# Kernel optimization log

Hardware: AMD Instinct MI355X
Metric: run time of the kernel (lower is better)

## Reference

```python
import jax, jax.numpy as jnp
import numpy as np
from jax import lax

EPS = 1e-4  # BatchNorm2d eps
K, STRIDE, PAD = 3, 1, 1


def _conv_nchw(x, w, stride, pad):
    return lax.conv_general_dilated(
        x, w, window_strides=(stride, stride), padding=[(pad, pad), (pad, pad)],
        dimension_numbers=("NCHW", "OIHW", "NCHW"))


def setup_inputs() -> dict:
    key = jax.random.key(0)
    ks = jax.random.split(key, 6)
    N, C, H, W = 16, 256, 56, 56
    Cout = 256
    return {
        "x": jax.random.normal(ks[0], (N, C, H, W), jnp.float32),
        "bn_gamma": jax.random.uniform(ks[1], (C,), jnp.float32, 0.5, 1.5),
        "bn_beta": jax.random.normal(ks[2], (C,), jnp.float32) * 0.1,
        "conv_w": jax.random.normal(ks[3], (Cout, C, K, K), jnp.float32) * (1.0 / np.sqrt(C * K * K)),
        "conv_b": jax.random.normal(ks[4], (Cout,), jnp.float32) * 0.01,
        "beta_conv_b": jax.random.normal(ks[5], (1,), jnp.float32) * 0.01,
    }


def reference(x, bn_gamma, bn_beta, conv_w, conv_b, beta_conv_b):
    # --- BatchNorm2d (training-mode batch stats, affine) ---
    mean = jnp.mean(x, axis=(0, 2, 3), keepdims=True)
    var = jnp.mean(jnp.square(x - mean), axis=(0, 2, 3), keepdims=True)  # biased
    xn = (x - mean) * lax.rsqrt(var + EPS)
    xn = xn * bn_gamma[None, :, None, None] + bn_beta[None, :, None, None]

    # --- Ternary quantize (threshold=0; le overwrites ge, so x==0 -> -1) ---
    t = jnp.where(xn >= 0.0, 1.0, 0.0)
    t = jnp.where(xn <= 0.0, -1.0, t).astype(xn.dtype)
    # scale=True, clamp=True
    xc = jnp.clip(xn, -1.0, 1.0)
    c_sum = jnp.sum(xc * t, axis=1, keepdims=True)       # [N,1,H,W]
    c_cnt = jnp.sum(jnp.abs(t), axis=1, keepdims=True)   # L1 norm over channels

    # --- Main conv on ternary activations ---
    y = _conv_nchw(t, conv_w, STRIDE, PAD) + conv_b[None, :, None, None]

    # --- beta: ones-weight box filter (+ beta_conv bias) ---
    ones_k = jnp.ones((1, 1, K, K), x.dtype)
    b_sum = _conv_nchw(c_sum, ones_k, STRIDE, PAD) + beta_conv_b[0]
    b_cnt = _conv_nchw(c_cnt, ones_k, STRIDE, PAD) + beta_conv_b[0]
    beta_map = b_sum / b_cnt                             # [N,1,Ho,Wo]
    return y * beta_map
```

## Files before the change

### kernel.cpp

```cpp
#include <hip/hip_runtime.h>
#include <hip/hip_bf16.h>

typedef __attribute__((ext_vector_type(8))) short bf16x8;
typedef __attribute__((ext_vector_type(4))) float f32x4;

#define NB 16
#define C 256
#define HH 56
#define WW 56
#define HW 3136
#define CHW 802816
#define NPIX 50176
#define PH 58
#define PW 58
#define KTOT 2304

#define GLL(g, l) __builtin_amdgcn_global_load_lds( \
    (const __attribute__((address_space(1))) void*)(g), \
    (__attribute__((address_space(3))) void*)(l), 16, 0, 0)

__global__ void stats_kernel(const float* __restrict__ x, const float* __restrict__ gamma,
                             double* __restrict__ stats) {
  int c = blockIdx.x, tid = threadIdx.x;
  double s = 0.0, s2 = 0.0;
  const float* xc = x + (size_t)c * HW;
  for (int n = 0; n < NB; ++n) {
    const float4* xb = (const float4*)(xc + (size_t)n * CHW);
    for (int i = tid; i < HW / 4; i += 256) {
      float4 v = xb[i];
      double a = v.x, b = v.y, cc = v.z, d = v.w;
      s  += (a + b) + (cc + d);
      s2 += (a * a + b * b) + (cc * cc + d * d);
    }
  }
  __shared__ double rs[256], rq[256];
  rs[tid] = s; rq[tid] = s2; __syncthreads();
  for (int o = 128; o > 0; o >>= 1) {
    if (tid < o) { rs[tid] += rs[tid + o]; rq[tid] += rq[tid + o]; }
    __syncthreads();
  }
  if (tid == 0) {
    double mean = rs[0] / (double)NPIX;
    double var = rq[0] / (double)NPIX - mean * mean;
    stats[c] = mean;
    stats[C + c] = (double)gamma[c] / sqrt(var + 1e-4);
  }
}

__global__ __launch_bounds__(256) void ternarize_kernel(const float* __restrict__ x,
                                 const float* __restrict__ beta,
                                 const double* __restrict__ stats,
                                 unsigned short* __restrict__ Tp, float* __restrict__ csum) {
  int bid = blockIdx.x, tid = threadIdx.x;
  int n = bid / HH, h = bid - n * HH;
  __shared__ float xs[256][57];
  const float* xb = x + (size_t)n * CHW + h * WW;
#pragma unroll
  for (int j = 0; j < 14; ++j) {
    int idx = j * 256 + tid;
    int c = idx / 14, q = idx - c * 14;
    float4 v = *(const float4*)(xb + (size_t)c * HW + q * 4);
    float* row = &xs[c][q * 4];
    row[0] = v.x; row[1] = v.y; row[2] = v.z; row[3] = v.w;
  }
  int c8 = tid & 31;
  double mu[8], sc[8], bt[8];
#pragma unroll
  for (int e = 0; e < 8; ++e) {
    int c = c8 + 32 * e;
    mu[e] = stats[c]; sc[e] = stats[C + c]; bt[e] = (double)beta[c];
  }
  __syncthreads();
  unsigned short* tb = Tp + ((size_t)(n * PH + h + 1) * PW + 1) * C;
  float* cs = csum + (size_t)(n * PH + h + 1) * PW + 1;
#pragma unroll
  for (int p = 0; p < 7; ++p) {
    int idx = p * 256 + tid;
    int w = idx >> 5;
    unsigned bits[4];
    float msum = 0.f;
#pragma unroll
    for (int e2 = 0; e2 < 4; ++e2) {
      unsigned lo, hi;
      {
        double xn = ((double)xs[c8 + 64 * e2][w] - mu[2 * e2]) * sc[2 * e2] + bt[2 * e2];
        lo = (xn > 0.0) ? 0x3F80u : 0xBF80u;
        msum += (float)fmin(fabs(xn), 1.0);
      }
      {
        double xn = ((double)xs[c8 + 64 * e2 + 32][w] - mu[2 * e2 + 1]) * sc[2 * e2 + 1] + bt[2 * e2 + 1];
        hi = (xn > 0.0) ? 0x3F80u : 0xBF80u;
        msum += (float)fmin(fabs(xn), 1.0);
      }
      bits[e2] = lo | (hi << 16);
    }
    msum += __shfl_xor(msum, 1); msum += __shfl_xor(msum, 2);
    msum += __shfl_xor(msum, 4); msum += __shfl_xor(msum, 8);
    msum += __shfl_xor(msum, 16);
    uint4 v4; v4.x = bits[0]; v4.y = bits[1]; v4.z = bits[2]; v4.w = bits[3];
    *(uint4*)(tb + (size_t)w * C + c8 * 8) = v4;
    if (c8 == 0) cs[w] = msum;
  }
}

__global__ void border_kernel(unsigned short* __restrict__ Tp) {
  int g = blockIdx.x * 256 + threadIdx.x;
  if (g >= 16 * 228 * 32) return;
  int n = g / 7296; int r = g - n * 7296;
  int pix = r >> 5, c8 = r & 31;
  int h, w;
  if (pix < 58)      { h = 0;  w = pix; }
  else if (pix < 116){ h = 57; w = pix - 58; }
  else { int rem = pix - 116; h = 1 + (rem >> 1); w = (rem & 1) ? 57 : 0; }
  uint4 z = {0u, 0u, 0u, 0u};
  *(uint4*)(Tp + (size_t)((n * PH + h) * PW + w) * C + c8 * 8) = z;
}

__global__ void wprep_kernel(const float* __restrict__ cw, unsigned short* __restrict__ Wp) {
  int o = blockIdx.x * 256 + threadIdx.x;
  int co = o / KTOT, rr = o - co * KTOT;
  int tap = rr >> 8, p = rr & 255;
  int c = (p & 7) * 32 + (p >> 3);
  float v = cw[co * KTOT + c * 9 + tap];
  unsigned u = __builtin_bit_cast(unsigned, v);
  unsigned lsb = (u >> 16) & 1u;
  u += 0x7FFFu + lsb;
  Wp[o] = (unsigned short)(u >> 16);
}

__global__ void betamap_kernel(const float* __restrict__ csum, const float* __restrict__ betab,
                               float* __restrict__ bmap) {
  int idx = blockIdx.x * 256 + threadIdx.x;
  if (idx >= NPIX) return;
  int n = idx / HW, r = idx - n * HW;
  int h = r / WW, w = r - h * WW;
  const float* p = csum + (size_t)(n * PH + h) * PW + w;
  float s = 0.f;
  for (int i = 0; i < 3; ++i)
    for (int j = 0; j < 3; ++j) s += p[i * PW + j];
  int rows = 3 - (h == 0) - (h == HH - 1);
  int cols = 3 - (w == 0) - (w == WW - 1);
  float bb = betab[0];
  bmap[idx] = (s + bb) / (256.0f * (float)(rows * cols) + bb);
}

__global__ __launch_bounds__(256) void conv_kernel(const unsigned short* __restrict__ Wp,
    const unsigned short* __restrict__ Tp, const float* __restrict__ convb,
    const float* __restrict__ bmap, float* __restrict__ out) {
  int g = blockIdx.x;
  int gg = g >> 3, xcd = g & 7;
  int ct = gg & 1;
  int pt = (gg >> 1) * 8 + xcd;
  int pix0 = pt * 128, co0 = ct * 128;
  int tid = threadIdx.x;

  __shared__ __align__(16) unsigned short As[128 * 64];
  __shared__ __align__(16) unsigned short Bs[128 * 64];

  int jj = tid & 7;
  int rr_ = tid >> 3;
  int s = ((jj ^ (rr_ & 7)) * 8);

  const unsigned short* wA[4];
  const unsigned short* tB[4];
  unsigned short* dA[4];
  unsigned short* dB[4];
#pragma unroll
  for (int i = 0; i < 4; ++i) {
    int r = i * 32 + rr_;
    wA[i] = Wp + (size_t)(co0 + r) * KTOT + s;
    dA[i] = As + i * 2048 + tid * 8;
    int p = pix0 + r;
    int n = p / HW; int rm = p - n * HW; int h = rm / WW; int w = rm - h * WW;
    tB[i] = Tp + (size_t)((n * PH + h) * PW + w) * C + s;
    dB[i] = Bs + i * 2048 + tid * 8;
  }

  int lane = tid & 63, wid = tid >> 6;
  int wm = (wid >> 1) * 64, wn = (wid & 1) * 64;
  int quad = lane >> 4, row16 = lane & 15;
  int j0 = quad ^ (row16 & 7);
  const unsigned short* aB0 = As + (wm + row16) * 64 + j0 * 8;
  const unsigned short* aB1 = As + (wm + row16) * 64 + (j0 ^ 4) * 8;
  const unsigned short* bB0 = Bs + (wn + row16) * 64 + j0 * 8;
  const unsigned short* bB1 = Bs + (wn + row16) * 64 + (j0 ^ 4) * 8;

  f32x4 acc[4][4];
#pragma unroll
  for (int mi = 0; mi < 4; ++mi)
#pragma unroll
    for (int ni = 0; ni < 4; ++ni)
      acc[mi][ni] = (f32x4){0.f, 0.f, 0.f, 0.f};

  for (int tap = 0; tap < 9; ++tap) {
    int kh = tap / 3, kw = tap - kh * 3;
    size_t aoff = (size_t)tap * 256;
    size_t boff = (size_t)(kh * PW + kw) * C;
#pragma unroll
    for (int c0 = 0; c0 < 256; c0 += 64) {
      __syncthreads();
#pragma unroll
      for (int i = 0; i < 4; ++i) GLL(wA[i] + aoff + c0, dA[i]);
#pragma unroll
      for (int i = 0; i < 4; ++i) GLL(tB[i] + boff + c0, dB[i]);
      __syncthreads();
#pragma unroll
      for (int kk = 0; kk < 2; ++kk) {
        const unsigned short* ap = kk ? aB1 : aB0;
        const unsigned short* bp = kk ? bB1 : bB0;
        bf16x8 a[4], b[4];
#pragma unroll
        for (int mi = 0; mi < 4; ++mi) a[mi] = *(const bf16x8*)(ap + mi * 1024);
#pragma unroll
        for (int ni = 0; ni < 4; ++ni) b[ni] = *(const bf16x8*)(bp + ni * 1024);
#pragma unroll
        for (int mi = 0; mi < 4; ++mi)
#pragma unroll
          for (int ni = 0; ni < 4; ++ni)
            acc[mi][ni] = __builtin_amdgcn_mfma_f32_16x16x32_bf16(a[mi], b[ni], acc[mi][ni], 0, 0, 0);
      }
    }
  }

#pragma unroll
  for (int ni = 0; ni < 4; ++ni) {
    int p = pix0 + wn + ni * 16 + row16;
    int n = p / HW; int r = p - n * HW;
    float bm = bmap[p];
    float* ob = out + (size_t)n * CHW + r;
#pragma unroll
    for (int mi = 0; mi < 4; ++mi) {
      int co = co0 + wm + mi * 16 + quad * 4;
#pragma unroll
      for (int rg = 0; rg < 4; ++rg) {
        ob[(size_t)(co + rg) * HW] = (acc[mi][ni][rg] + convb[co + rg]) * bm;
      }
    }
  }
}

extern "C" void kernel_launch(void* const* d_in, const int* in_sizes, int n_in,
                              void* d_out, int out_size, void* d_ws, size_t ws_size,
                              hipStream_t stream) {
  const float* x     = (const float*)d_in[0];
  const float* gamma = (const float*)d_in[1];
  const float* beta  = (const float*)d_in[2];
  const float* convw = (const float*)d_in[3];
  const float* convb = (const float*)d_in[4];
  const float* betab = (const float*)d_in[5];
  float* out = (float*)d_out;

  char* ws = (char*)d_ws;
  unsigned short* Tp   = (unsigned short*)(ws);
  unsigned short* Wp   = (unsigned short*)(ws + 27557888);
  float*          csum = (float*)(ws + 28737536);
  float*          bmap = (float*)(ws + 28952832);
  double*         stats= (double*)(ws + 29153536);

  hipMemsetAsync(csum, 0, 215296, stream);

  stats_kernel<<<256, 256, 0, stream>>>(x, gamma, stats);
  wprep_kernel<<<2304, 256, 0, stream>>>(convw, Wp);
  border_kernel<<<456, 256, 0, stream>>>(Tp);
  ternarize_kernel<<<896, 256, 0, stream>>>(x, beta, stats, Tp, csum);
  betamap_kernel<<<196, 256, 0, stream>>>(csum, betab, bmap);
  conv_kernel<<<784, 256, 0, stream>>>(Wp, Tp, convb, bmap, out);
}
```

Before: 225.7 us.

## Restructure conv to reuse shifted padded-pixel window across taps; merge prep kernels

The conv kernel now tiles over a contiguous window of padded-layout pixels and loads one channel slice of T once, so all nine taps read it from LDS at a constant pixel offset instead of reloading it per tap. Output columns on the padding ring are computed and then discarded. The tile becomes 64 output channels by 256 pixels, with a 32-channel K step that covers all nine taps per barrier. The weight, border and csum-zeroing prep work is merged into one launch, and the stats kernel uses 1024-thread blocks. The changes cut global T traffic and the number of launches, at the cost of some wasted MFMA work on padding pixels and a different LDS and register footprint.

```diff
diff --git a/kernel.cpp b/kernel.cpp
--- a/kernel.cpp
+++ b/kernel.cpp
@@ -14,28 +14,28 @@
 #define PH 58
 #define PW 58
 #define KTOT 2304
+#define PPI 3364
+#define NPIXP 53824
 
 #define GLL(g, l) __builtin_amdgcn_global_load_lds( \
     (const __attribute__((address_space(1))) void*)(g), \
     (__attribute__((address_space(3))) void*)(l), 16, 0, 0)
 
-__global__ void stats_kernel(const float* __restrict__ x, const float* __restrict__ gamma,
-                             double* __restrict__ stats) {
+__global__ __launch_bounds__(1024) void stats_kernel(const float* __restrict__ x,
+                             const float* __restrict__ gamma, double* __restrict__ stats) {
   int c = blockIdx.x, tid = threadIdx.x;
   double s = 0.0, s2 = 0.0;
   const float* xc = x + (size_t)c * HW;
-  for (int n = 0; n < NB; ++n) {
-    const float4* xb = (const float4*)(xc + (size_t)n * CHW);
-    for (int i = tid; i < HW / 4; i += 256) {
-      float4 v = xb[i];
-      double a = v.x, b = v.y, cc = v.z, d = v.w;
-      s  += (a + b) + (cc + d);
-      s2 += (a * a + b * b) + (cc * cc + d * d);
-    }
-  }
-  __shared__ double rs[256], rq[256];
+  for (int k = tid; k < NB * (HW / 4); k += 1024) {
+    int n = k / (HW / 4), i = k - n * (HW / 4);
+    float4 v = *(const float4*)(xc + (size_t)n * CHW + i * 4);
+    double a = v.x, b = v.y, cc = v.z, d = v.w;
+    s  += (a + b) + (cc + d);
+    s2 += (a * a + b * b) + (cc * cc + d * d);
+  }
+  __shared__ double rs[1024], rq[1024];
   rs[tid] = s; rq[tid] = s2; __syncthreads();
-  for (int o = 128; o > 0; o >>= 1) {
+  for (int o = 512; o > 0; o >>= 1) {
     if (tid < o) { rs[tid] += rs[tid + o]; rq[tid] += rq[tid + o]; }
     __syncthreads();
   }
@@ -103,29 +103,34 @@
   }
 }
 
-__global__ void border_kernel(unsigned short* __restrict__ Tp) {
-  int g = blockIdx.x * 256 + threadIdx.x;
-  if (g >= 16 * 228 * 32) return;
-  int n = g / 7296; int r = g - n * 7296;
-  int pix = r >> 5, c8 = r & 31;
-  int h, w;
-  if (pix < 58)      { h = 0;  w = pix; }
-  else if (pix < 116){ h = 57; w = pix - 58; }
-  else { int rem = pix - 116; h = 1 + (rem >> 1); w = (rem & 1) ? 57 : 0; }
-  uint4 z = {0u, 0u, 0u, 0u};
-  *(uint4*)(Tp + (size_t)((n * PH + h) * PW + w) * C + c8 * 8) = z;
-}
-
-__global__ void wprep_kernel(const float* __restrict__ cw, unsigned short* __restrict__ Wp) {
-  int o = blockIdx.x * 256 + threadIdx.x;
-  int co = o / KTOT, rr = o - co * KTOT;
-  int tap = rr >> 8, p = rr & 255;
-  int c = (p & 7) * 32 + (p >> 3);
-  float v = cw[co * KTOT + c * 9 + tap];
-  unsigned u = __builtin_bit_cast(unsigned, v);
-  unsigned lsb = (u >> 16) & 1u;
-  u += 0x7FFFu + lsb;
-  Wp[o] = (unsigned short)(u >> 16);
+__global__ void prep_kernel(const float* __restrict__ cw, unsigned short* __restrict__ Wp,
+                            unsigned short* __restrict__ Tp, float* __restrict__ csum) {
+  int b = blockIdx.x, tid = threadIdx.x;
+  if (b < 2304) {
+    int o = b * 256 + tid;
+    int co = o / KTOT, rr = o - co * KTOT;
+    int tap = rr >> 8, p = rr & 255;
+    int c = (p & 7) * 32 + (p >> 3);
+    float v = cw[co * KTOT + c * 9 + tap];
+    unsigned u = __builtin_bit_cast(unsigned, v);
+    unsigned lsb = (u >> 16) & 1u;
+    u += 0x7FFFu + lsb;
+    Wp[o] = (unsigned short)(u >> 16);
+  } else if (b < 2760) {
+    int g = (b - 2304) * 256 + tid;
+    if (g >= 16 * 228 * 32) return;
+    int n = g / 7296; int r = g - n * 7296;
+    int pix = r >> 5, c8 = r & 31;
+    int h, w;
+    if (pix < 58)      { h = 0;  w = pix; }
+    else if (pix < 116){ h = 57; w = pix - 58; }
+    else { int rem = pix - 116; h = 1 + (rem >> 1); w = (rem & 1) ? 57 : 0; }
+    uint4 z = {0u, 0u, 0u, 0u};
+    *(uint4*)(Tp + (size_t)((n * PH + h) * PW + w) * C + c8 * 8) = z;
+  } else {
+    int i = (b - 2760) * 256 + tid;
+    if (i < NPIXP) csum[i] = 0.f;
+  }
 }
 
 __global__ void betamap_kernel(const float* __restrict__ csum, const float* __restrict__ betab,
@@ -147,43 +152,37 @@
 __global__ __launch_bounds__(256) void conv_kernel(const unsigned short* __restrict__ Wp,
     const unsigned short* __restrict__ Tp, const float* __restrict__ convb,
     const float* __restrict__ bmap, float* __restrict__ out) {
-  int g = blockIdx.x;
-  int gg = g >> 3, xcd = g & 7;
-  int ct = gg & 1;
-  int pt = (gg >> 1) * 8 + xcd;
-  int pix0 = pt * 128, co0 = ct * 128;
+  int bid = blockIdx.x;
+  int ptg = bid >> 5, xcd = bid & 7, ct = (bid >> 3) & 3;
+  int pt = ptg * 8 + xcd;
+  if (pt >= 211) return;
   int tid = threadIdx.x;
-
-  __shared__ __align__(16) unsigned short As[128 * 64];
-  __shared__ __align__(16) unsigned short Bs[128 * 64];
-
-  int jj = tid & 7;
-  int rr_ = tid >> 3;
-  int s = ((jj ^ (rr_ & 7)) * 8);
-
-  const unsigned short* wA[4];
-  const unsigned short* tB[4];
-  unsigned short* dA[4];
-  unsigned short* dB[4];
-#pragma unroll
-  for (int i = 0; i < 4; ++i) {
-    int r = i * 32 + rr_;
-    wA[i] = Wp + (size_t)(co0 + r) * KTOT + s;
-    dA[i] = As + i * 2048 + tid * 8;
-    int p = pix0 + r;
-    int n = p / HW; int rm = p - n * HW; int h = rm / WW; int w = rm - h * WW;
-    tB[i] = Tp + (size_t)((n * PH + h) * PW + w) * C + s;
-    dB[i] = Bs + i * 2048 + tid * 8;
+  int co0 = ct * 64;
+  int pwin0 = pt * 256 - 64;
+
+  __shared__ __align__(16) unsigned short As[9 * 256 * 8];
+  __shared__ __align__(16) unsigned short Bs[384 * 36];
+
+  int aco = tid >> 2;
+  int asg = (tid & 3) ^ (aco & 3);
+  size_t aofs0 = (size_t)(co0 + aco) * KTOT + asg * 8;
+  unsigned short* adst0 = As + tid * 8;
+
+  int bofs[6]; unsigned short* bdst[6];
+#pragma unroll
+  for (int i = 0; i < 6; ++i) {
+    int lin = i * 256 + tid;
+    int pix = lin >> 2, sg = lin & 3;
+    int p = pwin0 + pix;
+    p = p < 0 ? 0 : (p >= NPIXP ? NPIXP - 1 : p);
+    bofs[i] = p * C + sg * 8;
+    bdst[i] = Bs + pix * 36 + sg * 8;
   }
 
   int lane = tid & 63, wid = tid >> 6;
-  int wm = (wid >> 1) * 64, wn = (wid & 1) * 64;
   int quad = lane >> 4, row16 = lane & 15;
-  int j0 = quad ^ (row16 & 7);
-  const unsigned short* aB0 = As + (wm + row16) * 64 + j0 * 8;
-  const unsigned short* aB1 = As + (wm + row16) * 64 + (j0 ^ 4) * 8;
-  const unsigned short* bB0 = Bs + (wn + row16) * 64 + j0 * 8;
-  const unsigned short* bB1 = Bs + (wn + row16) * 64 + (j0 ^ 4) * 8;
+  const unsigned short* aF = As + row16 * 32 + (quad ^ (row16 & 3)) * 8;
+  const unsigned short* bF = Bs + (wid * 64 + 64 + row16) * 36 + quad * 8;
 
   f32x4 acc[4][4];
 #pragma unroll
@@ -192,45 +191,46 @@
     for (int ni = 0; ni < 4; ++ni)
       acc[mi][ni] = (f32x4){0.f, 0.f, 0.f, 0.f};
 
-  for (int tap = 0; tap < 9; ++tap) {
-    int kh = tap / 3, kw = tap - kh * 3;
-    size_t aoff = (size_t)tap * 256;
-    size_t boff = (size_t)(kh * PW + kw) * C;
-#pragma unroll
-    for (int c0 = 0; c0 < 256; c0 += 64) {
-      __syncthreads();
-#pragma unroll
-      for (int i = 0; i < 4; ++i) GLL(wA[i] + aoff + c0, dA[i]);
-#pragma unroll
-      for (int i = 0; i < 4; ++i) GLL(tB[i] + boff + c0, dB[i]);
-      __syncthreads();
-#pragma unroll
-      for (int kk = 0; kk < 2; ++kk) {
-        const unsigned short* ap = kk ? aB1 : aB0;
-        const unsigned short* bp = kk ? bB1 : bB0;
-        bf16x8 a[4], b[4];
-#pragma unroll
-        for (int mi = 0; mi < 4; ++mi) a[mi] = *(const bf16x8*)(ap + mi * 1024);
-#pragma unroll
-        for (int ni = 0; ni < 4; ++ni) b[ni] = *(const bf16x8*)(bp + ni * 1024);
-#pragma unroll
-        for (int mi = 0; mi < 4; ++mi)
-#pragma unroll
-          for (int ni = 0; ni < 4; ++ni)
-            acc[mi][ni] = __builtin_amdgcn_mfma_f32_16x16x32_bf16(a[mi], b[ni], acc[mi][ni], 0, 0, 0);
-      }
+  for (int c0 = 0; c0 < 256; c0 += 32) {
+    __syncthreads();
+    uint4 breg[6];
+#pragma unroll
+    for (int i = 0; i < 6; ++i) breg[i] = *(const uint4*)(Tp + (size_t)bofs[i] + c0);
+#pragma unroll
+    for (int tap = 0; tap < 9; ++tap)
+      GLL(Wp + aofs0 + tap * 256 + c0, adst0 + tap * 2048);
+#pragma unroll
+    for (int i = 0; i < 6; ++i) *(uint4*)bdst[i] = breg[i];
+    __syncthreads();
+#pragma unroll
+    for (int tap = 0; tap < 9; ++tap) {
+      const int dt = (tap / 3 - 1) * PW + (tap % 3 - 1);
+      bf16x8 a[4], b[4];
+#pragma unroll
+      for (int mi = 0; mi < 4; ++mi) a[mi] = *(const bf16x8*)(aF + tap * 2048 + mi * 512);
+#pragma unroll
+      for (int ni = 0; ni < 4; ++ni) b[ni] = *(const bf16x8*)(bF + (ni * 16 + dt) * 36);
+#pragma unroll
+      for (int mi = 0; mi < 4; ++mi)
+#pragma unroll
+        for (int ni = 0; ni < 4; ++ni)
+          acc[mi][ni] = __builtin_amdgcn_mfma_f32_16x16x32_bf16(a[mi], b[ni], acc[mi][ni], 0, 0, 0);
     }
   }
 
 #pragma unroll
   for (int ni = 0; ni < 4; ++ni) {
-    int p = pix0 + wn + ni * 16 + row16;
-    int n = p / HW; int r = p - n * HW;
-    float bm = bmap[p];
-    float* ob = out + (size_t)n * CHW + r;
+    int pp = pt * 256 + wid * 64 + ni * 16 + row16;
+    if (pp >= NPIXP) continue;
+    int n = pp / PPI; int r = pp - n * PPI;
+    int ph = r / PW;  int pw = r - ph * PW;
+    if (ph < 1 || ph > 56 || pw < 1 || pw > 56) continue;
+    int pix = (ph - 1) * WW + (pw - 1);
+    float bm = bmap[n * HW + pix];
+    float* ob = out + (size_t)n * CHW + pix;
 #pragma unroll
     for (int mi = 0; mi < 4; ++mi) {
-      int co = co0 + wm + mi * 16 + quad * 4;
+      int co = co0 + mi * 16 + quad * 4;
 #pragma unroll
       for (int rg = 0; rg < 4; ++rg) {
         ob[(size_t)(co + rg) * HW] = (acc[mi][ni][rg] + convb[co + rg]) * bm;
@@ -257,12 +257,9 @@
   float*          bmap = (float*)(ws + 28952832);
   double*         stats= (double*)(ws + 29153536);
 
-  hipMemsetAsync(csum, 0, 215296, stream);
-
-  stats_kernel<<<256, 256, 0, stream>>>(x, gamma, stats);
-  wprep_kernel<<<2304, 256, 0, stream>>>(convw, Wp);
-  border_kernel<<<456, 256, 0, stream>>>(Tp);
+  prep_kernel<<<2971, 256, 0, stream>>>(convw, Wp, Tp, csum);
+  stats_kernel<<<256, 1024, 0, stream>>>(x, gamma, stats);
   ternarize_kernel<<<896, 256, 0, stream>>>(x, beta, stats, Tp, csum);
   betamap_kernel<<<196, 256, 0, stream>>>(csum, betab, bmap);
-  conv_kernel<<<784, 256, 0, stream>>>(Wp, Tp, convb, bmap, out);
-}
+  conv_kernel<<<864, 256, 0, stream>>>(Wp, Tp, convb, bmap, out);
+}
```

Measured after the change: 306.4 us. 35.7% more time.
